# Performance work log

Hardware: AMD Instinct MI355X
Metric: run time of the kernel (lower is better)

The kernel has to match this reference:

```python
import jax, jax.numpy as jnp
import numpy as np

B, H, L = 32768, 768, 10

def setup_inputs() -> dict:
    key = jax.random.key(0)
    ks = jax.random.split(key, 9)
    return {
        "hidden_state": jax.random.normal(ks[0], (B, H), dtype=jnp.float32),
        "w1": jax.random.normal(ks[1], (L, H), dtype=jnp.float32) * 0.02,
        "b1": jax.random.normal(ks[2], (L,), dtype=jnp.float32) * 0.02,
        "w2": jax.random.normal(ks[3], (L, H), dtype=jnp.float32) * 0.02,
        "b2": jax.random.normal(ks[4], (L,), dtype=jnp.float32) * 0.02,
        "w3": jax.random.normal(ks[5], (L, H), dtype=jnp.float32) * 0.02,
        "b3": jax.random.normal(ks[6], (L,), dtype=jnp.float32) * 0.02,
        "groups": jax.random.randint(ks[7], (B,), 0, 3, dtype=jnp.int32),
        "labels": jax.random.randint(ks[8], (B,), 0, L, dtype=jnp.int32),
    }

def reference(hidden_state, w1, b1, w2, b2, w3, b3, groups, labels):
    # Fused: run all 3 heads as one batched GEMM -> [B, 3, L]
    W = jnp.stack([w1, w2, w3])          # [3, L, H]
    bias = jnp.stack([b1, b2, b3])       # [3, L]
    logits3 = jnp.einsum('bh,glh->bgl', hidden_state, W) + bias[None, :, :]
    # Per-sample group selection (vectorized gather, replaces Python loop)
    logits = jnp.take_along_axis(logits3, groups[:, None, None].astype(jnp.int32), axis=1)[:, 0, :]  # [B, L]
    # Cross-entropy with mean reduction (nn.CrossEntropyLoss default)
    logp = jax.nn.log_softmax(logits, axis=-1)
    nll = -jnp.take_along_axis(logp, labels[:, None].astype(jnp.int32), axis=1)[:, 0]
    return jnp.mean(nll)
```

## Files before the change

### kernel.cpp

```cpp
#include <hip/hip_runtime.h>

#define B_N 32768
#define H_N 768
#define L_N 10
#define M_BLK 64
#define NCOL 32
#define NSLOT 96
#define KH_STEPS 12

typedef __attribute__((ext_vector_type(8))) short short8v;
typedef __attribute__((ext_vector_type(4))) float float4v;

static __device__ __forceinline__ short f2bf(float x) {
    unsigned u = __builtin_bit_cast(unsigned, x);
    u += 0x7fffu + ((u >> 16) & 1u);
    return (short)(u >> 16);
}

__global__ __launch_bounds__(512) void fused_mfma_ce(
    const float* __restrict__ hs,
    const float* __restrict__ w1, const float* __restrict__ b1v,
    const float* __restrict__ w2, const float* __restrict__ b2v,
    const float* __restrict__ w3, const float* __restrict__ b3v,
    const int* __restrict__ groups, const int* __restrict__ labels,
    float* __restrict__ out)
{
    __shared__ __align__(16) short wlds[NSLOT * NCOL * 8];

    const int t  = threadIdx.x;
    const int w  = t >> 6;
    const int mt = w & 3;
    const int kh = w >> 2;
    const int l  = t & 63;
    const int cq = l & 15;
    const int bq = l >> 4;

    for (int idx = t; idx < NCOL * NSLOT; idx += 512) {
        const int c    = idx / NSLOT;
        const int slot = idx % NSLOT;
        short8v v;
        if (c < 30) {
            const float* src = (c < 10) ? (w1 + c * H_N)
                             : (c < 20) ? (w2 + (c - 10) * H_N)
                                        : (w3 + (c - 20) * H_N);
            const float4 f0 = *reinterpret_cast<const float4*>(src + slot * 8);
            const float4 f1 = *reinterpret_cast<const float4*>(src + slot * 8 + 4);
            v[0] = f2bf(f0.x); v[1] = f2bf(f0.y); v[2] = f2bf(f0.z); v[3] = f2bf(f0.w);
            v[4] = f2bf(f1.x); v[5] = f2bf(f1.y); v[6] = f2bf(f1.z); v[7] = f2bf(f1.w);
        } else {
            v = short8v{0, 0, 0, 0, 0, 0, 0, 0};
        }
        *reinterpret_cast<short8v*>(wlds + (slot * NCOL + c) * 8) = v;
    }
    __syncthreads();

    const int m0 = blockIdx.x * M_BLK + mt * 16;
    const float* aptr = hs + (size_t)(m0 + cq) * H_N + kh * (H_N / 2) + bq * 8;
    const short* bb0 = wlds + (((kh * KH_STEPS * 4 + bq) * NCOL) + cq) * 8;
    const short* bb1 = bb0 + 16 * 8;

    float4v acc0 = {0.f, 0.f, 0.f, 0.f};
    float4v acc1 = {0.f, 0.f, 0.f, 0.f};

    #pragma unroll 4
    for (int ks = 0; ks < KH_STEPS; ++ks) {
        const float4 f0 = *reinterpret_cast<const float4*>(aptr + ks * 32);
        const float4 f1 = *reinterpret_cast<const float4*>(aptr + ks * 32 + 4);
        short8v a;
        a[0] = f2bf(f0.x); a[1] = f2bf(f0.y); a[2] = f2bf(f0.z); a[3] = f2bf(f0.w);
        a[4] = f2bf(f1.x); a[5] = f2bf(f1.y); a[6] = f2bf(f1.z); a[7] = f2bf(f1.w);
        const short8v b0 = *reinterpret_cast<const short8v*>(bb0 + ks * (NCOL * 4 * 8));
        const short8v b1 = *reinterpret_cast<const short8v*>(bb1 + ks * (NCOL * 4 * 8));
        acc0 = __builtin_amdgcn_mfma_f32_16x16x32_bf16(a, b0, acc0, 0, 0, 0);
        acc1 = __builtin_amdgcn_mfma_f32_16x16x32_bf16(a, b1, acc1, 0, 0, 0);
    }

    __syncthreads();
    float (*slog)[M_BLK][33] = (float (*)[M_BLK][33])wlds;
    #pragma unroll
    for (int r = 0; r < 4; ++r) {
        slog[kh][mt * 16 + bq * 4 + r][cq]      = acc0[r];
        slog[kh][mt * 16 + bq * 4 + r][cq + 16] = acc1[r];
    }
    __syncthreads();

    float nll = 0.f;
    if (t < M_BLK) {
        const int s   = blockIdx.x * M_BLK + t;
        const int g   = groups[s];
        const int lab = labels[s];
        const float* bp = (g == 0) ? b1v : ((g == 1) ? b2v : b3v);
        float lv[L_N];
        #pragma unroll
        for (int j = 0; j < L_N; ++j)
            lv[j] = slog[0][t][g * 10 + j] + slog[1][t][g * 10 + j] + bp[j];
        float m = lv[0];
        #pragma unroll
        for (int j = 1; j < L_N; ++j) m = fmaxf(m, lv[j]);
        float sum = 0.f;
        #pragma unroll
        for (int j = 0; j < L_N; ++j) sum += expf(lv[j] - m);
        float sel = lv[0];
        #pragma unroll
        for (int j = 1; j < L_N; ++j) sel = (lab == j) ? lv[j] : sel;
        nll = (m + logf(sum)) - sel;
    }
    if (t < 64) {
        #pragma unroll
        for (int off = 32; off > 0; off >>= 1)
            nll += __shfl_down(nll, off, 64);
        if (t == 0) atomicAdd(out, nll * (1.0f / (float)B_N));
    }
}

extern "C" void kernel_launch(void* const* d_in, const int* in_sizes, int n_in,
                              void* d_out, int out_size, void* d_ws, size_t ws_size,
                              hipStream_t stream) {
    const float* hs  = (const float*)d_in[0];
    const float* w1  = (const float*)d_in[1];
    const float* b1v = (const float*)d_in[2];
    const float* w2  = (const float*)d_in[3];
    const float* b2v = (const float*)d_in[4];
    const float* w3  = (const float*)d_in[5];
    const float* b3v = (const float*)d_in[6];
    const int* groups = (const int*)d_in[7];
    const int* labels = (const int*)d_in[8];
    float* out = (float*)d_out;

    hipMemsetAsync(out, 0, sizeof(float), stream);
    fused_mfma_ce<<<B_N / M_BLK, 512, 0, stream>>>(
        hs, w1, b1v, w2, b2v, w3, b3v, groups, labels, out);
}
```

Before: 32.36 us.

## Precompute bf16 weights in a prep kernel and split K four ways

Moves the per-block fp32-to-bf16 weight conversion and LDS staging into a separate prep kernel that writes packed bf16 weights to workspace. The main kernel then reads B fragments straight from global memory (L2-cached) and splits K across four wave groups with 32-row blocks, which doubles the grid and shortens each wave's K loop. It also swaps the manual rounding for the HIP bf16 pair-conversion intrinsic. This removes redundant per-block weight conversion and the LDS barrier, but adds a second kernel launch and a four-way partial-sum reduction in shared memory.

```diff
diff --git a/kernel.cpp b/kernel.cpp
--- a/kernel.cpp
+++ b/kernel.cpp
@@ -1,86 +1,88 @@
 #include <hip/hip_runtime.h>
+#include <hip/hip_bf16.h>
 
 #define B_N 32768
 #define H_N 768
 #define L_N 10
-#define M_BLK 64
+#define M_BLK 32
 #define NCOL 32
 #define NSLOT 96
-#define KH_STEPS 12
+#define KQ_STEPS 6
 
 typedef __attribute__((ext_vector_type(8))) short short8v;
 typedef __attribute__((ext_vector_type(4))) float float4v;
 
-static __device__ __forceinline__ short f2bf(float x) {
-    unsigned u = __builtin_bit_cast(unsigned, x);
-    u += 0x7fffu + ((u >> 16) & 1u);
-    return (short)(u >> 16);
+static __device__ __forceinline__ short8v cvt8(const float4 f0, const float4 f1) {
+    union { __hip_bfloat162 h[4]; short8v v; } u;
+    u.h[0] = __float22bfloat162_rn(make_float2(f0.x, f0.y));
+    u.h[1] = __float22bfloat162_rn(make_float2(f0.z, f0.w));
+    u.h[2] = __float22bfloat162_rn(make_float2(f1.x, f1.y));
+    u.h[3] = __float22bfloat162_rn(make_float2(f1.z, f1.w));
+    return u.v;
+}
+
+__global__ __launch_bounds__(256) void prep_weights(
+    const float* __restrict__ w1, const float* __restrict__ w2,
+    const float* __restrict__ w3, short* __restrict__ wb)
+{
+    const int idx = blockIdx.x * 256 + threadIdx.x;
+    if (idx >= NSLOT * NCOL) return;
+    const int slot = idx >> 5;
+    const int c    = idx & 31;
+    short8v v;
+    if (c < 30) {
+        const float* src = (c < 10) ? (w1 + c * H_N)
+                         : (c < 20) ? (w2 + (c - 10) * H_N)
+                                    : (w3 + (c - 20) * H_N);
+        const float4 f0 = *reinterpret_cast<const float4*>(src + slot * 8);
+        const float4 f1 = *reinterpret_cast<const float4*>(src + slot * 8 + 4);
+        v = cvt8(f0, f1);
+    } else {
+        v = short8v{0, 0, 0, 0, 0, 0, 0, 0};
+    }
+    *reinterpret_cast<short8v*>(wb + idx * 8) = v;
 }
 
 __global__ __launch_bounds__(512) void fused_mfma_ce(
-    const float* __restrict__ hs,
-    const float* __restrict__ w1, const float* __restrict__ b1v,
-    const float* __restrict__ w2, const float* __restrict__ b2v,
-    const float* __restrict__ w3, const float* __restrict__ b3v,
+    const float* __restrict__ hs, const short* __restrict__ wb,
+    const float* __restrict__ b1v, const float* __restrict__ b2v,
+    const float* __restrict__ b3v,
     const int* __restrict__ groups, const int* __restrict__ labels,
     float* __restrict__ out)
 {
-    __shared__ __align__(16) short wlds[NSLOT * NCOL * 8];
+    __shared__ float slog[4][M_BLK][33];
 
     const int t  = threadIdx.x;
     const int w  = t >> 6;
-    const int mt = w & 3;
-    const int kh = w >> 2;
+    const int mt = w & 1;
+    const int kq = w >> 1;
     const int l  = t & 63;
     const int cq = l & 15;
     const int bq = l >> 4;
 
-    for (int idx = t; idx < NCOL * NSLOT; idx += 512) {
-        const int c    = idx / NSLOT;
-        const int slot = idx % NSLOT;
-        short8v v;
-        if (c < 30) {
-            const float* src = (c < 10) ? (w1 + c * H_N)
-                             : (c < 20) ? (w2 + (c - 10) * H_N)
-                                        : (w3 + (c - 20) * H_N);
-            const float4 f0 = *reinterpret_cast<const float4*>(src + slot * 8);
-            const float4 f1 = *reinterpret_cast<const float4*>(src + slot * 8 + 4);
-            v[0] = f2bf(f0.x); v[1] = f2bf(f0.y); v[2] = f2bf(f0.z); v[3] = f2bf(f0.w);
-            v[4] = f2bf(f1.x); v[5] = f2bf(f1.y); v[6] = f2bf(f1.z); v[7] = f2bf(f1.w);
-        } else {
-            v = short8v{0, 0, 0, 0, 0, 0, 0, 0};
-        }
-        *reinterpret_cast<short8v*>(wlds + (slot * NCOL + c) * 8) = v;
-    }
-    __syncthreads();
-
     const int m0 = blockIdx.x * M_BLK + mt * 16;
-    const float* aptr = hs + (size_t)(m0 + cq) * H_N + kh * (H_N / 2) + bq * 8;
-    const short* bb0 = wlds + (((kh * KH_STEPS * 4 + bq) * NCOL) + cq) * 8;
+    const float* aptr = hs + (size_t)(m0 + cq) * H_N + kq * (H_N / 4) + bq * 8;
+    const short* bb0 = wb + (((kq * KQ_STEPS * 4 + bq) * NCOL) + cq) * 8;
     const short* bb1 = bb0 + 16 * 8;
 
     float4v acc0 = {0.f, 0.f, 0.f, 0.f};
     float4v acc1 = {0.f, 0.f, 0.f, 0.f};
 
-    #pragma unroll 4
-    for (int ks = 0; ks < KH_STEPS; ++ks) {
+    #pragma unroll 2
+    for (int ks = 0; ks < KQ_STEPS; ++ks) {
         const float4 f0 = *reinterpret_cast<const float4*>(aptr + ks * 32);
         const float4 f1 = *reinterpret_cast<const float4*>(aptr + ks * 32 + 4);
-        short8v a;
-        a[0] = f2bf(f0.x); a[1] = f2bf(f0.y); a[2] = f2bf(f0.z); a[3] = f2bf(f0.w);
-        a[4] = f2bf(f1.x); a[5] = f2bf(f1.y); a[6] = f2bf(f1.z); a[7] = f2bf(f1.w);
         const short8v b0 = *reinterpret_cast<const short8v*>(bb0 + ks * (NCOL * 4 * 8));
         const short8v b1 = *reinterpret_cast<const short8v*>(bb1 + ks * (NCOL * 4 * 8));
+        const short8v a = cvt8(f0, f1);
         acc0 = __builtin_amdgcn_mfma_f32_16x16x32_bf16(a, b0, acc0, 0, 0, 0);
         acc1 = __builtin_amdgcn_mfma_f32_16x16x32_bf16(a, b1, acc1, 0, 0, 0);
     }
 
-    __syncthreads();
-    float (*slog)[M_BLK][33] = (float (*)[M_BLK][33])wlds;
     #pragma unroll
     for (int r = 0; r < 4; ++r) {
-        slog[kh][mt * 16 + bq * 4 + r][cq]      = acc0[r];
-        slog[kh][mt * 16 + bq * 4 + r][cq + 16] = acc1[r];
+        slog[kq][mt * 16 + bq * 4 + r][cq]      = acc0[r];
+        slog[kq][mt * 16 + bq * 4 + r][cq + 16] = acc1[r];
     }
     __syncthreads();
 
@@ -93,7 +95,8 @@
         float lv[L_N];
         #pragma unroll
         for (int j = 0; j < L_N; ++j)
-            lv[j] = slog[0][t][g * 10 + j] + slog[1][t][g * 10 + j] + bp[j];
+            lv[j] = slog[0][t][g * 10 + j] + slog[1][t][g * 10 + j]
+                  + slog[2][t][g * 10 + j] + slog[3][t][g * 10 + j] + bp[j];
         float m = lv[0];
         #pragma unroll
         for (int j = 1; j < L_N; ++j) m = fmaxf(m, lv[j]);
@@ -126,8 +129,10 @@
     const int* groups = (const int*)d_in[7];
     const int* labels = (const int*)d_in[8];
     float* out = (float*)d_out;
+    short* wb  = (short*)d_ws;
 
     hipMemsetAsync(out, 0, sizeof(float), stream);
+    prep_weights<<<(NSLOT * NCOL + 255) / 256, 256, 0, stream>>>(w1, w2, w3, wb);
     fused_mfma_ce<<<B_N / M_BLK, 512, 0, stream>>>(
-        hs, w1, b1v, w2, b2v, w3, b3v, groups, labels, out);
+        hs, wb, b1v, b2v, b3v, groups, labels, out);
 }
```

Result: slower. 36.04 us (+11.4%).
